# Kernel optimization log

Hardware: AMD Instinct MI355X
Metric: run time of the kernel (lower is better)

The kernel has to match this reference:

```python
import jax, jax.numpy as jnp
import numpy as np

WS = 8   # window_size
SS = 4   # shift_size
NH = 12  # num_heads
DIM = 384
HD = DIM // NH


def _rel_index():
    coords = np.stack(np.meshgrid(np.arange(WS), np.arange(WS), indexing='ij'))  # (2, ws, ws)
    cf = coords.reshape(2, -1)                       # (2, n)
    rel = (cf[:, :, None] - cf[:, None, :]).transpose(1, 2, 0).copy()  # (n, n, 2)
    rel[..., 0] += WS - 1
    rel[..., 1] += WS - 1
    rel[..., 0] *= 2 * WS - 1
    return rel.sum(-1)                               # (n, n) int


def _attn_mask(h, w):
    img = np.zeros((h, w))
    sl = (slice(0, -WS), slice(-WS, -SS), slice(-SS, None))
    cnt = 0
    for hs in sl:
        for ws_ in sl:
            img[hs, ws_] = cnt
            cnt += 1
    mw = img.reshape(h // WS, WS, w // WS, WS).transpose(0, 2, 1, 3).reshape(-1, WS * WS)  # (nW, n)
    d = mw[:, None, :] - mw[:, :, None]
    return np.where(d != 0, -100.0, 0.0).astype(np.float32)  # (nW, n, n)


def setup_inputs() -> dict:
    key = jax.random.key(0)
    ks = jax.random.split(key, 10)
    B, H, W = 32, 64, 64
    std = 0.02
    return {
        'x': jax.random.normal(ks[0], (B, H, W, DIM), jnp.float32),
        'wq': jax.random.normal(ks[1], (DIM, DIM), jnp.float32) * std,
        'bq': jnp.zeros((DIM,), jnp.float32),
        'wk': jax.random.normal(ks[2], (DIM, DIM), jnp.float32) * std,
        'bk': jnp.zeros((DIM,), jnp.float32),
        'wv': jax.random.normal(ks[3], (DIM, DIM), jnp.float32) * std,
        'bv': jnp.zeros((DIM,), jnp.float32),
        'wo': jax.random.normal(ks[4], (DIM, DIM), jnp.float32) * std,
        'bo': jnp.zeros((DIM,), jnp.float32),
        'bias_table': jax.random.normal(ks[5], ((2 * WS - 1) ** 2, NH), jnp.float32) * std,
    }


def reference(x, wq, bq, wk, bk, wv, bv, wo, bo, bias_table):
    b, h, w, c = x.shape
    pad_h = (-h) % WS
    pad_w = (-w) % WS
    if pad_h or pad_w:
        x = jnp.pad(x, ((0, 0), (0, pad_h), (0, pad_w), (0, 0)))
    hp, wp = x.shape[1], x.shape[2]

    if SS > 0:
        x_sh = jnp.roll(x, shift=(-SS, -SS), axis=(1, 2))
        mask = jnp.asarray(_attn_mask(hp, wp))          # (nW, n, n)
    else:
        x_sh = x
        mask = None

    # window partition -> (B*nW, n, C)
    nwh, nww = hp // WS, wp // WS
    win = x_sh.reshape(b, nwh, WS, nww, WS, c).transpose(0, 1, 3, 2, 4, 5)
    win = win.reshape(-1, WS * WS, c)
    b_, n, _ = win.shape

    scale = HD ** -0.5
    q = (win @ wq.T + bq).reshape(b_, n, NH, HD).transpose(0, 2, 1, 3) * scale
    k = (win @ wk.T + bk).reshape(b_, n, NH, HD).transpose(0, 2, 1, 3)
    v = (win @ wv.T + bv).reshape(b_, n, NH, HD).transpose(0, 2, 1, 3)

    attn = jnp.einsum('bhnd,bhmd->bhnm', q, k)          # (b_, NH, n, n)
    rel = bias_table[jnp.asarray(_rel_index()).reshape(-1)].reshape(n, n, NH)
    attn = attn + rel.transpose(2, 0, 1)[None]
    if mask is not None:
        nW = mask.shape[0]
        attn = attn.reshape(b_ // nW, nW, NH, n, n) + mask[None, :, None]
        attn = attn.reshape(b_, NH, n, n)
    attn = jax.nn.softmax(attn, axis=-1)

    out = jnp.einsum('bhnm,bhmd->bhnd', attn, v).transpose(0, 2, 1, 3).reshape(b_, n, c)
    out = out @ wo.T + bo

    # window reverse -> (B, hp, wp, C)
    out = out.reshape(b, nwh, nww, WS, WS, c).transpose(0, 1, 3, 2, 4, 5).reshape(b, hp, wp, c)
    if SS > 0:
        out = jnp.roll(out, shift=(SS, SS), axis=(1, 2))
    return out[:, :h, :w, :]
```

## Files before the change

### kernel.cpp

```cpp
#include <hip/hip_runtime.h>
#include <hip/hip_bf16.h>

typedef short bf16x8 __attribute__((ext_vector_type(8)));
typedef float f32x4 __attribute__((ext_vector_type(4)));

#define NH_ 12
#define DIM_ 384

static __device__ __forceinline__ float bf2f_us(ushort u) {
    __hip_bfloat16 h; __builtin_memcpy(&h, &u, 2);
    return __bfloat162float(h);
}
static __device__ __forceinline__ ushort f2us(float f) {
    __hip_bfloat16 h = __float2bfloat16(f);
    ushort u; __builtin_memcpy(&u, &h, 2);
    return u;
}

static __device__ __forceinline__ void gload_lds16(const void* g, void* l) {
    __builtin_amdgcn_global_load_lds(
        (const __attribute__((address_space(1))) unsigned int*)g,
        (__attribute__((address_space(3))) unsigned int*)l, 16, 0, 0);
}

static __device__ __forceinline__ int regioncnt(int t, int wr, int wc) {
    int rr = (wr == 7) ? (((t >> 3) < 4) ? 1 : 2) : 0;
    int cc = (wc == 7) ? (((t & 7) < 4) ? 1 : 2) : 0;
    return rr * 3 + cc;
}

__global__ __launch_bounds__(256) void convert_kernel(
    const float* wq, const float* wk, const float* wv, const float* wo,
    const float* bq, const float* bk, const float* bv, const float* bo,
    const float* bt, ushort* __restrict__ dst)
{
    const int N = 594060;
    for (int i = blockIdx.x * 256 + threadIdx.x; i < N; i += gridDim.x * 256) {
        const float* src; int off;
        if (i < 589824) {
            int wsel = i / 147456; off = i - wsel * 147456;
            src = (wsel == 0) ? wq : (wsel == 1) ? wk : (wsel == 2) ? wv : wo;
        } else if (i < 591360) {
            int bsel = (i - 589824) / 384; off = (i - 589824) - bsel * 384;
            src = (bsel == 0) ? bq : (bsel == 1) ? bk : (bsel == 2) ? bv : bo;
        } else {
            off = i - 591360; src = bt;
        }
        dst[i] = f2us(src[off]);
    }
}

__global__ __launch_bounds__(256) void bias_kernel(
    const ushort* __restrict__ tablec, float* __restrict__ biasv)
{
    const int vh = blockIdx.x;
    const int v = vh / NH_, h = vh - v * NH_;
    const int wr = (v & 2) ? 7 : 0, wc = (v & 1) ? 7 : 0;
    const int tid = threadIdx.x, lane = tid & 63;
    #pragma unroll
    for (int i = 0; i < 4; ++i) {
        const int tno = (tid >> 6) + 4 * i;
        const int rt = tno >> 2, ct = tno & 3;
        const int jj = ct * 16 + (lane & 15);
        const int cntj = regioncnt(jj, wr, wc);
        float4 o;
        float vals[4];
        #pragma unroll
        for (int r = 0; r < 4; ++r) {
            const int ii = rt * 16 + (lane >> 4) * 4 + r;
            const int idx = ((ii >> 3) - (jj >> 3) + 7) * 15 + ((ii & 7) - (jj & 7) + 7);
            float val = bf2f_us(tablec[idx * NH_ + h]);
            if (regioncnt(ii, wr, wc) != cntj) val -= 100.f;
            vals[r] = val;
        }
        o.x = vals[0]; o.y = vals[1]; o.z = vals[2]; o.w = vals[3];
        reinterpret_cast<float4*>(biasv)[((size_t)vh * 16 + tno) * 64 + lane] = o;
    }
}

__global__ __launch_bounds__(256, 4) void qkv_gemm(
    const float* __restrict__ x, const ushort* __restrict__ wb,
    ushort* __restrict__ qws, ushort* __restrict__ kws, ushort* __restrict__ vws,
    int wbase, int nmb)
{
    __shared__ __align__(16) ushort As[2][4096];
    __shared__ __align__(16) ushort Bs[2][4096];
    const int nwg = nmb * 9;
    const int orig = blockIdx.x;
    const int wgid = (orig & 7) * (nwg >> 3) + (orig >> 3);
    const int mb = wgid / 9, nt = wgid - mb * 9;
    const int wsel = nt / 3, ntm = nt - wsel * 3;
    const int n0 = nt * 128;
    const int tid = threadIdx.x, lane = tid & 63, wv = tid >> 6;
    const int col16 = lane & 15, quad = lane >> 4;
    const int wm = wv >> 1, wn = wv & 1;

    const int kofA = ((tid >> 5) & 3) * 8 + (tid & 1) * 4;
    const float* arow[4];
    #pragma unroll
    for (int it = 0; it < 4; ++it) {
        const int row = (it * 2 + (tid >> 7)) * 16 + ((tid >> 1) & 15);
        const int wglob = wbase + mb * 2 + (row >> 6);
        const int token = row & 63;
        const int b = wglob >> 6, widx = wglob & 63, wr = widx >> 3, wc = widx & 7;
        const int orr = (wr * 8 + (token >> 3) + 4) & 63;
        const int occ = (wc * 8 + (token & 7) + 4) & 63;
        arow[it] = x + (((size_t)b * 64 + orr) * 64 + occ) * DIM_ + kofA;
    }

    const ushort* bsrc = wb + (size_t)n0 * DIM_;
    const int brow_l = lane & 15, bkof = (lane >> 4) * 8;

    f32x4 acc[4][4];
    #pragma unroll
    for (int i2 = 0; i2 < 4; ++i2)
        #pragma unroll
        for (int j2 = 0; j2 < 4; ++j2)
            acc[i2][j2] = (f32x4){0.f, 0.f, 0.f, 0.f};

    const int NK = DIM_ / 32;

    #pragma unroll
    for (int c2 = 0; c2 < 2; ++c2) {
        const int blk = wv * 2 + c2;
        gload_lds16(bsrc + (size_t)(blk * 16 + brow_l) * DIM_ + bkof, &Bs[0][blk * 512]);
    }
    #pragma unroll
    for (int it = 0; it < 4; ++it) {
        const float4 v = *reinterpret_cast<const float4*>(arow[it]);
        ushort4 u4; u4.x = f2us(v.x); u4.y = f2us(v.y); u4.z = f2us(v.z); u4.w = f2us(v.w);
        *reinterpret_cast<ushort4*>(&As[0][it * 1024 + tid * 4]) = u4;
    }
    __syncthreads();

    for (int t = 0; t < NK; ++t) {
        const int cur = t & 1, nxt = cur ^ 1;
        const int kk = t * 32;
        float4 av[4];
        if (t + 1 < NK) {
            #pragma unroll
            for (int it = 0; it < 4; ++it)
                av[it] = *reinterpret_cast<const float4*>(arow[it] + kk + 32);
            #pragma unroll
            for (int c2 = 0; c2 < 2; ++c2) {
                const int blk = wv * 2 + c2;
                gload_lds16(bsrc + (size_t)(blk * 16 + brow_l) * DIM_ + kk + 32 + bkof,
                            &Bs[nxt][blk * 512]);
            }
        }
        bf16x8 af[4], bfm[4];
        #pragma unroll
        for (int rt = 0; rt < 4; ++rt)
            af[rt] = *reinterpret_cast<const bf16x8*>(&As[cur][(wm * 4 + rt) * 512 + lane * 8]);
        #pragma unroll
        for (int ct = 0; ct < 4; ++ct)
            bfm[ct] = *reinterpret_cast<const bf16x8*>(&Bs[cur][(wn * 4 + ct) * 512 + lane * 8]);
        #pragma unroll
        for (int rt = 0; rt < 4; ++rt)
            #pragma unroll
            for (int ct = 0; ct < 4; ++ct)
                acc[rt][ct] = __builtin_amdgcn_mfma_f32_16x16x32_bf16(af[rt], bfm[ct], acc[rt][ct], 0, 0, 0);
        if (t + 1 < NK) {
            #pragma unroll
            for (int it = 0; it < 4; ++it) {
                ushort4 u4;
                u4.x = f2us(av[it].x); u4.y = f2us(av[it].y);
                u4.z = f2us(av[it].z); u4.w = f2us(av[it].w);
                *reinterpret_cast<ushort4*>(&As[nxt][it * 1024 + tid * 4]) = u4;
            }
        }
        __syncthreads();
    }

    const int lw = mb * 2 + wm;
    const float scale = 0.17677669529663687f;
    const ushort* bias_all = wb + 589824 + wsel * 384;
    #pragma unroll
    for (int ct = 0; ct < 4; ++ct) {
        const int jl = ntm * 128 + wn * 64 + ct * 16 + col16;
        const int head = jl >> 5, hd = jl & 31;
        const float bj = bf2f_us(bias_all[jl]);
        #pragma unroll
        for (int rt = 0; rt < 4; ++rt) {
            if (wsel == 2) {
                ushort4 pk;
                pk.x = f2us(acc[rt][ct][0] + bj);
                pk.y = f2us(acc[rt][ct][1] + bj);
                pk.z = f2us(acc[rt][ct][2] + bj);
                pk.w = f2us(acc[rt][ct][3] + bj);
                *reinterpret_cast<ushort4*>(
                    vws + ((size_t)(lw * NH_ + head) * 32 + hd) * 64 + rt * 16 + quad * 4) = pk;
            } else {
                #pragma unroll
                for (int r = 0; r < 4; ++r) {
                    const int token = rt * 16 + quad * 4 + r;
                    const float v = acc[rt][ct][r] + bj;
                    if (wsel == 0)
                        qws[((size_t)(lw * NH_ + head) * 64 + token) * 32 + hd] = f2us(v * scale);
                    else
                        kws[((size_t)(lw * NH_ + head) * 64 + token) * 32 + hd] = f2us(v);
                }
            }
        }
    }
}

__global__ __launch_bounds__(256) void attn_kernel(
    const __hip_bfloat16* __restrict__ qws, const __hip_bfloat16* __restrict__ kws,
    const __hip_bfloat16* __restrict__ vws, const float* __restrict__ biasv,
    __hip_bfloat16* __restrict__ attnout, int wbase)
{
    __shared__ __align__(16) ushort Pbuf[4][64 * 72];
    const int bid = blockIdx.x;
    const int lw = bid / 3, hg = bid - lw * 3;
    const int tid = threadIdx.x, wvi = tid >> 6, lane = tid & 63;
    const int h = hg * 4 + wvi;
    const int w = wbase + lw;
    const int col16 = lane & 15, quad = lane >> 4;
    const ushort* qp = reinterpret_cast<const ushort*>(qws) + ((size_t)lw * NH_ + h) * 64 * 32;
    const ushort* kp = reinterpret_cast<const ushort*>(kws) + ((size_t)lw * NH_ + h) * 64 * 32;
    const ushort* vp = reinterpret_cast<const ushort*>(vws) + ((size_t)lw * NH_ + h) * 32 * 64;

    bf16x8 aq[4], bk4[4];
    #pragma unroll
    for (int t = 0; t < 4; ++t) {
        aq[t]  = *reinterpret_cast<const bf16x8*>(qp + (t * 16 + col16) * 32 + quad * 8);
        bk4[t] = *reinterpret_cast<const bf16x8*>(kp + (t * 16 + col16) * 32 + quad * 8);
    }
    f32x4 S[4][4];
    #pragma unroll
    for (int rt = 0; rt < 4; ++rt) {
        #pragma unroll
        for (int ct = 0; ct < 4; ++ct) {
            f32x4 z = {0.f,0.f,0.f,0.f};
            S[rt][ct] = __builtin_amdgcn_mfma_f32_16x16x32_bf16(aq[rt], bk4[ct], z, 0, 0, 0);
        }
    }

    const int widx = w & 63, wr = widx >> 3, wc = widx & 7;
    const int v = ((wr == 7) ? 2 : 0) + ((wc == 7) ? 1 : 0);
    const float4* bp = reinterpret_cast<const float4*>(biasv) +
                       ((size_t)(v * NH_ + h) * 16) * 64 + lane;
    #pragma unroll
    for (int rt = 0; rt < 4; ++rt) {
        #pragma unroll
        for (int ct = 0; ct < 4; ++ct) {
            const float4 bb = bp[(rt * 4 + ct) * 64];
            S[rt][ct][0] += bb.x; S[rt][ct][1] += bb.y;
            S[rt][ct][2] += bb.z; S[rt][ct][3] += bb.w;
        }
    }

    ushort* pb_w = &Pbuf[wvi][0];
    #pragma unroll
    for (int rt = 0; rt < 4; ++rt) {
        float rm[4], rs[4];
        #pragma unroll
        for (int r = 0; r < 4; ++r)
            rm[r] = fmaxf(fmaxf(S[rt][0][r], S[rt][1][r]), fmaxf(S[rt][2][r], S[rt][3][r]));
        #pragma unroll
        for (int d = 1; d <= 8; d <<= 1) {
            #pragma unroll
            for (int r = 0; r < 4; ++r) rm[r] = fmaxf(rm[r], __shfl_xor(rm[r], d, 64));
        }
        #pragma unroll
        for (int r = 0; r < 4; ++r) rs[r] = 0.f;
        #pragma unroll
        for (int ct = 0; ct < 4; ++ct) {
            #pragma unroll
            for (int r = 0; r < 4; ++r) {
                float p = __expf(S[rt][ct][r] - rm[r]);
                S[rt][ct][r] = p;
                rs[r] += p;
            }
        }
        #pragma unroll
        for (int d = 1; d <= 8; d <<= 1) {
            #pragma unroll
            for (int r = 0; r < 4; ++r) rs[r] += __shfl_xor(rs[r], d, 64);
        }
        #pragma unroll
        for (int ct = 0; ct < 4; ++ct) {
            #pragma unroll
            for (int r = 0; r < 4; ++r) {
                const float inv = 1.0f / rs[r];
                pb_w[(rt * 16 + quad * 4 + r) * 72 + ct * 16 + col16] =
                    f2us(S[rt][ct][r] * inv);
            }
        }
    }

    f32x4 O[4][2];
    #pragma unroll
    for (int rt = 0; rt < 4; ++rt) {
        f32x4 z = {0.f,0.f,0.f,0.f};
        O[rt][0] = z; O[rt][1] = z;
    }
    #pragma unroll
    for (int ks = 0; ks < 2; ++ks) {
        bf16x8 bv0 = *reinterpret_cast<const bf16x8*>(vp + (col16)*64 + ks * 32 + quad * 8);
        bf16x8 bv1 = *reinterpret_cast<const bf16x8*>(vp + (16 + col16) * 64 + ks * 32 + quad * 8);
        #pragma unroll
        for (int rt = 0; rt < 4; ++rt) {
            bf16x8 ap = *reinterpret_cast<const bf16x8*>(pb_w + (rt * 16 + col16) * 72 + ks * 32 + quad * 8);
            O[rt][0] = __builtin_amdgcn_mfma_f32_16x16x32_bf16(ap, bv0, O[rt][0], 0, 0, 0);
            O[rt][1] = __builtin_amdgcn_mfma_f32_16x16x32_bf16(ap, bv1, O[rt][1], 0, 0, 0);
        }
    }
    __hip_bfloat16* op = attnout + (size_t)lw * 64 * DIM_ + h * 32;
    #pragma unroll
    for (int rt = 0; rt < 4; ++rt) {
        #pragma unroll
        for (int c2 = 0; c2 < 2; ++c2) {
            #pragma unroll
            for (int r = 0; r < 4; ++r) {
                const int token = rt * 16 + quad * 4 + r;
                op[token * DIM_ + c2 * 16 + col16] = __float2bfloat16(O[rt][c2][r]);
            }
        }
    }
}

__global__ __launch_bounds__(256, 4) void proj_gemm(
    const ushort* __restrict__ attnin, const ushort* __restrict__ wb,
    float* __restrict__ out, int wbase, int nmb)
{
    __shared__ __align__(16) ushort As[2][4096];
    __shared__ __align__(16) ushort Bs[2][4096];
    const int nwg = nmb * 3;
    const int orig = blockIdx.x;
    const int wgid = (orig & 7) * (nwg >> 3) + (orig >> 3);
    const int mb = wgid / 3, nt = wgid - mb * 3;
    const int n0 = nt * 128;
    const int tid = threadIdx.x, lane = tid & 63, wv = tid >> 6;
    const int col16 = lane & 15, quad = lane >> 4;
    const int wm = wv >> 1, wn = wv & 1;

    const ushort* asrc = attnin + (size_t)mb * 128 * DIM_;
    const ushort* bsrc = wb + (size_t)3 * 147456 + (size_t)n0 * DIM_;
    const int row_l = lane & 15, kof_l = (lane >> 4) * 8;

    f32x4 acc[4][4];
    #pragma unroll
    for (int i2 = 0; i2 < 4; ++i2)
        #pragma unroll
        for (int j2 = 0; j2 < 4; ++j2)
            acc[i2][j2] = (f32x4){0.f, 0.f, 0.f, 0.f};

    const int NK = DIM_ / 32;

    #pragma unroll
    for (int c2 = 0; c2 < 2; ++c2) {
        const int blk = wv * 2 + c2;
        gload_lds16(asrc + (size_t)(blk * 16 + row_l) * DIM_ + kof_l, &As[0][blk * 512]);
        gload_lds16(bsrc + (size_t)(blk * 16 + row_l) * DIM_ + kof_l, &Bs[0][blk * 512]);
    }
    __syncthreads();

    for (int t = 0; t < NK; ++t) {
        const int cur = t & 1, nxt = cur ^ 1;
        const int kk = t * 32;
        if (t + 1 < NK) {
            #pragma unroll
            for (int c2 = 0; c2 < 2; ++c2) {
                const int blk = wv * 2 + c2;
                gload_lds16(asrc + (size_t)(blk * 16 + row_l) * DIM_ + kk + 32 + kof_l,
                            &As[nxt][blk * 512]);
                gload_lds16(bsrc + (size_t)(blk * 16 + row_l) * DIM_ + kk + 32 + kof_l,
                            &Bs[nxt][blk * 512]);
            }
        }
        bf16x8 af[4], bfm[4];
        #pragma unroll
        for (int rt = 0; rt < 4; ++rt)
            af[rt] = *reinterpret_cast<const bf16x8*>(&As[cur][(wm * 4 + rt) * 512 + lane * 8]);
        #pragma unroll
        for (int ct = 0; ct < 4; ++ct)
            bfm[ct] = *reinterpret_cast<const bf16x8*>(&Bs[cur][(wn * 4 + ct) * 512 + lane * 8]);
        #pragma unroll
        for (int rt = 0; rt < 4; ++rt)
            #pragma unroll
            for (int ct = 0; ct < 4; ++ct)
                acc[rt][ct] = __builtin_amdgcn_mfma_f32_16x16x32_bf16(af[rt], bfm[ct], acc[rt][ct], 0, 0, 0);
        __syncthreads();
    }

    const int lw = mb * 2 + wm;
    const int wglob = wbase + lw;
    const int b = wglob >> 6, widx = wglob & 63, wr = widx >> 3, wc = widx & 7;
    const ushort* boc = wb + 589824 + 3 * 384;
    #pragma unroll
    for (int ct = 0; ct < 4; ++ct) {
        const int j = n0 + wn * 64 + ct * 16 + col16;
        const float bj = bf2f_us(boc[j]);
        #pragma unroll
        for (int rt = 0; rt < 4; ++rt) {
            #pragma unroll
            for (int r = 0; r < 4; ++r) {
                const int token = rt * 16 + quad * 4 + r;
                const int orr = (wr * 8 + (token >> 3) + 4) & 63;
                const int occ = (wc * 8 + (token & 7) + 4) & 63;
                out[(((size_t)b * 64 + orr) * 64 + occ) * DIM_ + j] = acc[rt][ct][r] + bj;
            }
        }
    }
}

extern "C" void kernel_launch(void* const* d_in, const int* in_sizes, int n_in,
                              void* d_out, int out_size, void* d_ws, size_t ws_size,
                              hipStream_t stream) {
    const float* x = (const float*)d_in[0];
    float* out = (float*)d_out;
    char* ws = (char*)d_ws;

    ushort* wb    = (ushort*)ws;
    float*  biasv = (float*)(ws + 1188352);
    const size_t FIXED = 1974784;

    int wchunk = 128;
    const int cands[4] = {2048, 1024, 512, 256};
    for (int i = 0; i < 4; ++i) {
        if (FIXED + (size_t)cands[i] * 4 * 49152 <= ws_size) { wchunk = cands[i]; break; }
    }
    const size_t CQ = (size_t)wchunk * NH_ * 64 * 32 * 2;
    __hip_bfloat16* qws = (__hip_bfloat16*)(ws + FIXED);
    __hip_bfloat16* kws = (__hip_bfloat16*)(ws + FIXED + CQ);
    __hip_bfloat16* vws = (__hip_bfloat16*)(ws + FIXED + 2 * CQ);
    __hip_bfloat16* att = (__hip_bfloat16*)(ws + FIXED + 3 * CQ);

    convert_kernel<<<dim3(512), dim3(256), 0, stream>>>(
        (const float*)d_in[1], (const float*)d_in[3], (const float*)d_in[5], (const float*)d_in[7],
        (const float*)d_in[2], (const float*)d_in[4], (const float*)d_in[6], (const float*)d_in[8],
        (const float*)d_in[9], wb);
    bias_kernel<<<dim3(48), dim3(256), 0, stream>>>(wb + 591360, biasv);

    for (int c = 0; c < 2048 / wchunk; ++c) {
        const int wbase = c * wchunk;
        const int nmb = wchunk / 2;
        qkv_gemm<<<dim3(nmb * 9), dim3(256), 0, stream>>>(
            x, wb, (ushort*)qws, (ushort*)kws, (ushort*)vws, wbase, nmb);
        attn_kernel<<<dim3(wchunk * 3), dim3(256), 0, stream>>>(
            qws, kws, vws, biasv, att, wbase);
        proj_gemm<<<dim3(nmb * 3), dim3(256), 0, stream>>>(
            (const ushort*)att, wb, out, wbase, nmb);
    }
}
```

Measured before the change: 867.5 us.

## Pre-tile activations and weights into MFMA layout and triple-buffer GEMM loads

Adds an xprep kernel that gathers the shifted window tokens from x, converts them to bf16 and writes them in a tile-major layout that matches the MFMA fragments. The convert kernel and the attention output use the same tiled layout, so both GEMMs can stream A and B with contiguous direct-to-LDS loads. The GEMM main loops move from a two-buffer to a three-buffer LDS pipeline with explicit vmcnt waits and raw barriers. This removes the per-tile fp32 A conversion and strided gathers from qkv_gemm, at the cost of one extra kernel and an extra bf16 round trip of x through memory, plus lower occupancy from the larger LDS footprint.

```diff
diff --git a/kernel.cpp b/kernel.cpp
--- a/kernel.cpp
+++ b/kernel.cpp
@@ -29,6 +29,7 @@
     return rr * 3 + cc;
 }
 
+
 __global__ __launch_bounds__(256) void convert_kernel(
     const float* wq, const float* wk, const float* wv, const float* wo,
     const float* bq, const float* bk, const float* bv, const float* bo,
@@ -36,17 +37,29 @@
 {
     const int N = 594060;
     for (int i = blockIdx.x * 256 + threadIdx.x; i < N; i += gridDim.x * 256) {
-        const float* src; int off;
         if (i < 589824) {
-            int wsel = i / 147456; off = i - wsel * 147456;
-            src = (wsel == 0) ? wq : (wsel == 1) ? wk : (wsel == 2) ? wv : wo;
+            const int nt12 = i / 49152;
+            const int j = i - nt12 * 49152;
+            const int t = j >> 12, rb = (j >> 9) & 7, l = (j >> 3) & 63, e = j & 7;
+            const int row128 = rb * 16 + (l & 15);
+            const int k = t * 32 + ((l >> 4) << 3) + e;
+            const float* src; int row;
+            if (nt12 < 9) {
+                const int wsel = nt12 / 3;
+                src = (wsel == 0) ? wq : (wsel == 1) ? wk : wv;
+                row = (nt12 - wsel * 3) * 128 + row128;
+            } else {
+                src = wo; row = (nt12 - 9) * 128 + row128;
+            }
+            dst[i] = f2us(src[row * 384 + k]);
         } else if (i < 591360) {
-            int bsel = (i - 589824) / 384; off = (i - 589824) - bsel * 384;
-            src = (bsel == 0) ? bq : (bsel == 1) ? bk : (bsel == 2) ? bv : bo;
+            const int bsel = (i - 589824) / 384;
+            const int off = (i - 589824) - bsel * 384;
+            const float* src = (bsel == 0) ? bq : (bsel == 1) ? bk : (bsel == 2) ? bv : bo;
+            dst[i] = f2us(src[off]);
         } else {
-            off = i - 591360; src = bt;
-        }
-        dst[i] = f2us(src[off]);
+            dst[i] = f2us(bt[i - 591360]);
+        }
     }
 }
 
@@ -78,38 +91,48 @@
     }
 }
 
-__global__ __launch_bounds__(256, 4) void qkv_gemm(
-    const float* __restrict__ x, const ushort* __restrict__ wb,
+__global__ __launch_bounds__(256) void xprep_kernel(
+    const float* __restrict__ x, ushort* __restrict__ xc, int wbase, int nmb)
+{
+    const int mb = blockIdx.x;
+    const int tid = threadIdx.x;
+    ushort* outp = xc + (size_t)mb * 49152;
+    #pragma unroll 4
+    for (int it = 0; it < 48; ++it) {
+        const int g = it * 256 + tid;
+        const int row = g / 96, f4 = g - row * 96;
+        const int wglob = wbase + mb * 2 + (row >> 6);
+        const int token = row & 63;
+        const int b = wglob >> 6, widx = wglob & 63, wr = widx >> 3, wc = widx & 7;
+        const int orr = (wr * 8 + (token >> 3) + 4) & 63;
+        const int occ = (wc * 8 + (token & 7) + 4) & 63;
+        const float4 v = *reinterpret_cast<const float4*>(
+            x + (((size_t)b * 64 + orr) * 64 + occ) * DIM_ + f4 * 4);
+        ushort4 u4; u4.x = f2us(v.x); u4.y = f2us(v.y); u4.z = f2us(v.z); u4.w = f2us(v.w);
+        const int idx = (f4 >> 3) * 4096 + (row >> 4) * 512 +
+                        ((f4 >> 1) & 3) * 128 + (row & 15) * 8 + (f4 & 1) * 4;
+        *reinterpret_cast<ushort4*>(outp + idx) = u4;
+    }
+}
+
+__global__ __launch_bounds__(256, 3) void qkv_gemm(
+    const ushort* __restrict__ xc, const ushort* __restrict__ wb,
     ushort* __restrict__ qws, ushort* __restrict__ kws, ushort* __restrict__ vws,
-    int wbase, int nmb)
-{
-    __shared__ __align__(16) ushort As[2][4096];
-    __shared__ __align__(16) ushort Bs[2][4096];
+    int nmb)
+{
+    __shared__ __align__(16) ushort As[3][4096];
+    __shared__ __align__(16) ushort Bs[3][4096];
     const int nwg = nmb * 9;
     const int orig = blockIdx.x;
     const int wgid = (orig & 7) * (nwg >> 3) + (orig >> 3);
     const int mb = wgid / 9, nt = wgid - mb * 9;
     const int wsel = nt / 3, ntm = nt - wsel * 3;
-    const int n0 = nt * 128;
     const int tid = threadIdx.x, lane = tid & 63, wv = tid >> 6;
     const int col16 = lane & 15, quad = lane >> 4;
     const int wm = wv >> 1, wn = wv & 1;
 
-    const int kofA = ((tid >> 5) & 3) * 8 + (tid & 1) * 4;
-    const float* arow[4];
-    #pragma unroll
-    for (int it = 0; it < 4; ++it) {
-        const int row = (it * 2 + (tid >> 7)) * 16 + ((tid >> 1) & 15);
-        const int wglob = wbase + mb * 2 + (row >> 6);
-        const int token = row & 63;
-        const int b = wglob >> 6, widx = wglob & 63, wr = widx >> 3, wc = widx & 7;
-        const int orr = (wr * 8 + (token >> 3) + 4) & 63;
-        const int occ = (wc * 8 + (token & 7) + 4) & 63;
-        arow[it] = x + (((size_t)b * 64 + orr) * 64 + occ) * DIM_ + kofA;
-    }
-
-    const ushort* bsrc = wb + (size_t)n0 * DIM_;
-    const int brow_l = lane & 15, bkof = (lane >> 4) * 8;
+    const ushort* asrc = xc + (size_t)mb * 49152 + lane * 8;
+    const ushort* bsrc = wb + (size_t)nt * 49152 + lane * 8;
 
     f32x4 acc[4][4];
     #pragma unroll
@@ -118,36 +141,22 @@
         for (int j2 = 0; j2 < 4; ++j2)
             acc[i2][j2] = (f32x4){0.f, 0.f, 0.f, 0.f};
 
-    const int NK = DIM_ / 32;
-
-    #pragma unroll
-    for (int c2 = 0; c2 < 2; ++c2) {
-        const int blk = wv * 2 + c2;
-        gload_lds16(bsrc + (size_t)(blk * 16 + brow_l) * DIM_ + bkof, &Bs[0][blk * 512]);
-    }
-    #pragma unroll
-    for (int it = 0; it < 4; ++it) {
-        const float4 v = *reinterpret_cast<const float4*>(arow[it]);
-        ushort4 u4; u4.x = f2us(v.x); u4.y = f2us(v.y); u4.z = f2us(v.z); u4.w = f2us(v.w);
-        *reinterpret_cast<ushort4*>(&As[0][it * 1024 + tid * 4]) = u4;
-    }
-    __syncthreads();
-
-    for (int t = 0; t < NK; ++t) {
-        const int cur = t & 1, nxt = cur ^ 1;
-        const int kk = t * 32;
-        float4 av[4];
-        if (t + 1 < NK) {
-            #pragma unroll
-            for (int it = 0; it < 4; ++it)
-                av[it] = *reinterpret_cast<const float4*>(arow[it] + kk + 32);
-            #pragma unroll
-            for (int c2 = 0; c2 < 2; ++c2) {
-                const int blk = wv * 2 + c2;
-                gload_lds16(bsrc + (size_t)(blk * 16 + brow_l) * DIM_ + kk + 32 + bkof,
-                            &Bs[nxt][blk * 512]);
-            }
-        }
+    #define STAGE(T, BUF)                                                        \
+        gload_lds16(asrc + (T)*4096 + (2*wv)*512,   &As[BUF][(2*wv)*512]);       \
+        gload_lds16(asrc + (T)*4096 + (2*wv+1)*512, &As[BUF][(2*wv+1)*512]);     \
+        gload_lds16(bsrc + (T)*4096 + (2*wv)*512,   &Bs[BUF][(2*wv)*512]);       \
+        gload_lds16(bsrc + (T)*4096 + (2*wv+1)*512, &Bs[BUF][(2*wv+1)*512]);
+
+    STAGE(0, 0)
+    STAGE(1, 1)
+
+    #pragma unroll
+    for (int t = 0; t < 12; ++t) {
+        if (t < 11) asm volatile("s_waitcnt vmcnt(4)" ::: "memory");
+        else        asm volatile("s_waitcnt vmcnt(0)" ::: "memory");
+        __builtin_amdgcn_s_barrier();
+        if (t < 10) { STAGE(t + 2, (t + 2) % 3) }
+        const int cur = t % 3;
         bf16x8 af[4], bfm[4];
         #pragma unroll
         for (int rt = 0; rt < 4; ++rt)
@@ -160,17 +169,9 @@
             #pragma unroll
             for (int ct = 0; ct < 4; ++ct)
                 acc[rt][ct] = __builtin_amdgcn_mfma_f32_16x16x32_bf16(af[rt], bfm[ct], acc[rt][ct], 0, 0, 0);
-        if (t + 1 < NK) {
-            #pragma unroll
-            for (int it = 0; it < 4; ++it) {
-                ushort4 u4;
-                u4.x = f2us(av[it].x); u4.y = f2us(av[it].y);
-                u4.z = f2us(av[it].z); u4.w = f2us(av[it].w);
-                *reinterpret_cast<ushort4*>(&As[nxt][it * 1024 + tid * 4]) = u4;
-            }
-        }
-        __syncthreads();
-    }
+        asm volatile("s_waitcnt lgkmcnt(0)" ::: "memory");
+    }
+    #undef STAGE
 
     const int lw = mb * 2 + wm;
     const float scale = 0.17677669529663687f;
@@ -208,7 +209,7 @@
 __global__ __launch_bounds__(256) void attn_kernel(
     const __hip_bfloat16* __restrict__ qws, const __hip_bfloat16* __restrict__ kws,
     const __hip_bfloat16* __restrict__ vws, const float* __restrict__ biasv,
-    __hip_bfloat16* __restrict__ attnout, int wbase)
+    ushort* __restrict__ attnout, int wbase)
 {
     __shared__ __align__(16) ushort Pbuf[4][64 * 72];
     const int bid = blockIdx.x;
@@ -307,38 +308,37 @@
             O[rt][1] = __builtin_amdgcn_mfma_f32_16x16x32_bf16(ap, bv1, O[rt][1], 0, 0, 0);
         }
     }
-    __hip_bfloat16* op = attnout + (size_t)lw * 64 * DIM_ + h * 32;
+    ushort* op = attnout + (size_t)(lw >> 1) * 49152 + (size_t)h * 4096 + (lw & 1) * 2048;
+    const int elo = col16 & 7;
     #pragma unroll
     for (int rt = 0; rt < 4; ++rt) {
         #pragma unroll
         for (int c2 = 0; c2 < 2; ++c2) {
+            const int kch = c2 * 2 + (col16 >> 3);
             #pragma unroll
             for (int r = 0; r < 4; ++r) {
-                const int token = rt * 16 + quad * 4 + r;
-                op[token * DIM_ + c2 * 16 + col16] = __float2bfloat16(O[rt][c2][r]);
-            }
-        }
-    }
-}
-
-__global__ __launch_bounds__(256, 4) void proj_gemm(
+                op[rt * 512 + kch * 128 + (quad * 4 + r) * 8 + elo] = f2us(O[rt][c2][r]);
+            }
+        }
+    }
+}
+
+__global__ __launch_bounds__(256, 3) void proj_gemm(
     const ushort* __restrict__ attnin, const ushort* __restrict__ wb,
     float* __restrict__ out, int wbase, int nmb)
 {
-    __shared__ __align__(16) ushort As[2][4096];
-    __shared__ __align__(16) ushort Bs[2][4096];
+    __shared__ __align__(16) ushort As[3][4096];
+    __shared__ __align__(16) ushort Bs[3][4096];
     const int nwg = nmb * 3;
     const int orig = blockIdx.x;
     const int wgid = (orig & 7) * (nwg >> 3) + (orig >> 3);
     const int mb = wgid / 3, nt = wgid - mb * 3;
-    const int n0 = nt * 128;
     const int tid = threadIdx.x, lane = tid & 63, wv = tid >> 6;
     const int col16 = lane & 15, quad = lane >> 4;
     const int wm = wv >> 1, wn = wv & 1;
 
-    const ushort* asrc = attnin + (size_t)mb * 128 * DIM_;
-    const ushort* bsrc = wb + (size_t)3 * 147456 + (size_t)n0 * DIM_;
-    const int row_l = lane & 15, kof_l = (lane >> 4) * 8;
+    const ushort* asrc = attnin + (size_t)mb * 49152 + lane * 8;
+    const ushort* bsrc = wb + (size_t)(9 + nt) * 49152 + lane * 8;
 
     f32x4 acc[4][4];
     #pragma unroll
@@ -347,29 +347,22 @@
         for (int j2 = 0; j2 < 4; ++j2)
             acc[i2][j2] = (f32x4){0.f, 0.f, 0.f, 0.f};
 
-    const int NK = DIM_ / 32;
-
-    #pragma unroll
-    for (int c2 = 0; c2 < 2; ++c2) {
-        const int blk = wv * 2 + c2;
-        gload_lds16(asrc + (size_t)(blk * 16 + row_l) * DIM_ + kof_l, &As[0][blk * 512]);
-        gload_lds16(bsrc + (size_t)(blk * 16 + row_l) * DIM_ + kof_l, &Bs[0][blk * 512]);
-    }
-    __syncthreads();
-
-    for (int t = 0; t < NK; ++t) {
-        const int cur = t & 1, nxt = cur ^ 1;
-        const int kk = t * 32;
-        if (t + 1 < NK) {
-            #pragma unroll
-            for (int c2 = 0; c2 < 2; ++c2) {
-                const int blk = wv * 2 + c2;
-                gload_lds16(asrc + (size_t)(blk * 16 + row_l) * DIM_ + kk + 32 + kof_l,
-                            &As[nxt][blk * 512]);
-                gload_lds16(bsrc + (size_t)(blk * 16 + row_l) * DIM_ + kk + 32 + kof_l,
-                            &Bs[nxt][blk * 512]);
-            }
-        }
+    #define STAGE(T, BUF)                                                        \
+        gload_lds16(asrc + (T)*4096 + (2*wv)*512,   &As[BUF][(2*wv)*512]);       \
+        gload_lds16(asrc + (T)*4096 + (2*wv+1)*512, &As[BUF][(2*wv+1)*512]);     \
+        gload_lds16(bsrc + (T)*4096 + (2*wv)*512,   &Bs[BUF][(2*wv)*512]);       \
+        gload_lds16(bsrc + (T)*4096 + (2*wv+1)*512, &Bs[BUF][(2*wv+1)*512]);
+
+    STAGE(0, 0)
+    STAGE(1, 1)
+
+    #pragma unroll
+    for (int t = 0; t < 12; ++t) {
+        if (t < 11) asm volatile("s_waitcnt vmcnt(4)" ::: "memory");
+        else        asm volatile("s_waitcnt vmcnt(0)" ::: "memory");
+        __builtin_amdgcn_s_barrier();
+        if (t < 10) { STAGE(t + 2, (t + 2) % 3) }
+        const int cur = t % 3;
         bf16x8 af[4], bfm[4];
         #pragma unroll
         for (int rt = 0; rt < 4; ++rt)
@@ -382,8 +375,9 @@
             #pragma unroll
             for (int ct = 0; ct < 4; ++ct)
                 acc[rt][ct] = __builtin_amdgcn_mfma_f32_16x16x32_bf16(af[rt], bfm[ct], acc[rt][ct], 0, 0, 0);
-        __syncthreads();
-    }
+        asm volatile("s_waitcnt lgkmcnt(0)" ::: "memory");
+    }
+    #undef STAGE
 
     const int lw = mb * 2 + wm;
     const int wglob = wbase + lw;
@@ -391,7 +385,7 @@
     const ushort* boc = wb + 589824 + 3 * 384;
     #pragma unroll
     for (int ct = 0; ct < 4; ++ct) {
-        const int j = n0 + wn * 64 + ct * 16 + col16;
+        const int j = nt * 128 + wn * 64 + ct * 16 + col16;
         const float bj = bf2f_us(boc[j]);
         #pragma unroll
         for (int rt = 0; rt < 4; ++rt) {
@@ -422,11 +416,11 @@
     for (int i = 0; i < 4; ++i) {
         if (FIXED + (size_t)cands[i] * 4 * 49152 <= ws_size) { wchunk = cands[i]; break; }
     }
-    const size_t CQ = (size_t)wchunk * NH_ * 64 * 32 * 2;
-    __hip_bfloat16* qws = (__hip_bfloat16*)(ws + FIXED);
-    __hip_bfloat16* kws = (__hip_bfloat16*)(ws + FIXED + CQ);
-    __hip_bfloat16* vws = (__hip_bfloat16*)(ws + FIXED + 2 * CQ);
-    __hip_bfloat16* att = (__hip_bfloat16*)(ws + FIXED + 3 * CQ);
+    const size_t CQ = (size_t)wchunk * 49152;
+    ushort* xcatt = (ushort*)(ws + FIXED);
+    ushort* qws   = (ushort*)(ws + FIXED + CQ);
+    ushort* kws   = (ushort*)(ws + FIXED + 2 * CQ);
+    ushort* vws   = (ushort*)(ws + FIXED + 3 * CQ);
 
     convert_kernel<<<dim3(512), dim3(256), 0, stream>>>(
         (const float*)d_in[1], (const float*)d_in[3], (const float*)d_in[5], (const float*)d_in[7],
@@ -437,11 +431,13 @@
     for (int c = 0; c < 2048 / wchunk; ++c) {
         const int wbase = c * wchunk;
         const int nmb = wchunk / 2;
+        xprep_kernel<<<dim3(nmb), dim3(256), 0, stream>>>(x, xcatt, wbase, nmb);
         qkv_gemm<<<dim3(nmb * 9), dim3(256), 0, stream>>>(
-            x, wb, (ushort*)qws, (ushort*)kws, (ushort*)vws, wbase, nmb);
+            xcatt, wb, qws, kws, vws, nmb);
         attn_kernel<<<dim3(wchunk * 3), dim3(256), 0, stream>>>(
-            qws, kws, vws, biasv, att, wbase);
+            (const __hip_bfloat16*)qws, (const __hip_bfloat16*)kws,
+            (const __hip_bfloat16*)vws, biasv, xcatt, wbase);
         proj_gemm<<<dim3(nmb * 3), dim3(256), 0, stream>>>(
-            (const ushort*)att, wb, out, wbase, nmb);
-    }
-}
+            xcatt, wb, out, wbase, nmb);
+    }
+}
```

New measurement: 786.0 us. 1.1x faster.
